# Performance work log

Hardware: AMD Instinct MI355X
Metric: run time of the kernel (lower is better)

The kernel has to match this reference:

```python
import jax, jax.numpy as jnp
import numpy as np

LEAK_VALUE = 0.1
B, N_ATOMS, IN_F, H, MAX_VAL, OUT_F = 256, 128, 128, 256, 6, 256


def gru(x, W_ih, W_hh, b_ih, b_hh):
    # x: [B, T, in]; W_ih: [3H, in]; W_hh: [3H, H]; gate order r,z,n (torch)
    Bb, T, _ = x.shape
    Hh = W_hh.shape[1]
    x_proj = jnp.einsum('bti,gi->btg', x, W_ih) + b_ih  # [B, T, 3H]

    def step(h, xp):
        gh = h @ W_hh.T + b_hh                      # [B, 3H]
        xr, xz, xn = jnp.split(xp, 3, axis=-1)
        hr, hz, hn = jnp.split(gh, 3, axis=-1)
        r = jax.nn.sigmoid(xr + hr)
        z = jax.nn.sigmoid(xz + hz)
        n = jnp.tanh(xn + r * hn)
        h_new = (1.0 - z) * n + z * h
        return h_new, h_new

    h0 = jnp.zeros((Bb, Hh), x.dtype)
    _, out = jax.lax.scan(step, h0, jnp.swapaxes(x_proj, 0, 1))  # [T, B, H]
    return jnp.swapaxes(out, 0, 1)  # [B, T, H]


def setup_inputs() -> dict:
    key = jax.random.key(0)
    ks = jax.random.split(key, 8)
    s = 0.05
    return {
        'x': jax.random.normal(ks[0], (B, N_ATOMS, IN_F), jnp.float32),
        'bonded_atoms': jax.random.randint(ks[1], (B, N_ATOMS, MAX_VAL), 0, N_ATOMS),
        'W_ih': jax.random.normal(ks[2], (3 * H, IN_F), jnp.float32) * s,
        'W_hh': jax.random.normal(ks[3], (3 * H, H), jnp.float32) * s,
        'b_ih': jax.random.normal(ks[4], (3 * H,), jnp.float32) * s,
        'b_hh': jax.random.normal(ks[5], (3 * H,), jnp.float32) * s,
        'W_fc': jax.random.normal(ks[6], (OUT_F, H * MAX_VAL), jnp.float32) * s,
        'b_fc': jax.random.normal(ks[7], (OUT_F,), jnp.float32) * s,
    }


def reference(x, bonded_atoms, W_ih, W_hh, b_ih, b_hh, W_fc, b_fc):
    rnn_out = gru(x, W_ih, W_hh, b_ih, b_hh)               # [B, N, H]
    batch_idx = jnp.arange(x.shape[0])[:, None, None]       # [B, 1, 1]
    fc_in = rnn_out[batch_idx, bonded_atoms]                # [B, N, V, H] gather
    fc_in = fc_in.reshape(x.shape[0], x.shape[1], -1)       # [B, N, V*H]
    out = fc_in @ W_fc.T + b_fc                             # [B, N, OUT_F]
    return jnp.where(out >= 0, out, LEAK_VALUE * out)
```

## Files before the change

kernel.cpp:

```cpp
#include <hip/hip_runtime.h>
#include <hip/hip_bf16.h>
#include <stdint.h>

typedef unsigned short u16;
typedef __bf16 bf16_t;
typedef bf16_t bf16x8 __attribute__((ext_vector_type(8)));
typedef u16    u16x8  __attribute__((ext_vector_type(8)));
typedef u16    u16x4  __attribute__((ext_vector_type(4)));
typedef float  f32x4  __attribute__((ext_vector_type(4)));

#define BSZ    256
#define NATOMS 128
#define INF    128
#define HH     256
#define H3     768
#define MAXV   6
#define OUTF   256
#define KFC    (HH * MAXV)
#define PLANE  8388608
#define HAP    264

__device__ __forceinline__ u16 f2bf(float f) {
  union { float f; unsigned u; } v; v.f = f;
  unsigned u = v.u;
  unsigned r = (u + 0x7FFFu + ((u >> 16) & 1u)) >> 16;
  return (u16)r;
}
__device__ __forceinline__ float bf2f(u16 h) {
  union { unsigned u; float f; } v; v.u = ((unsigned)h) << 16;
  return v.f;
}
__device__ __forceinline__ f32x4 mfma_bf16(u16x8 a, u16x8 b, f32x4 c) {
  return __builtin_amdgcn_mfma_f32_16x16x32_bf16(
      __builtin_bit_cast(bf16x8, a), __builtin_bit_cast(bf16x8, b), c, 0, 0, 0);
}
__device__ __forceinline__ float sel4(float a0, float a1, float a2, float a3, int q) {
  float t01 = (q & 1) ? a1 : a0;
  float t23 = (q & 1) ? a3 : a2;
  return (q & 2) ? t23 : t01;
}

#define NX4   1048576
#define C1    1048576
#define C2    1073152
#define C3    1122304
#define C4    1220608
__global__ void k_prep4(const float* __restrict__ x, const float* __restrict__ wih,
                        const float* __restrict__ whh, const float* __restrict__ wfc,
                        u16* __restrict__ xb, u16* __restrict__ wihb,
                        u16* __restrict__ whhb, u16* __restrict__ wfcb) {
  int i = blockIdx.x * 256 + threadIdx.x;
  const float* src; u16* dst; int j;
  if (i < C1)      { src = x;   dst = xb;   j = i; }
  else if (i < C2) { src = wih; dst = wihb; j = i - C1; }
  else if (i < C3) { src = whh; dst = whhb; j = i - C2; }
  else             { src = wfc; dst = wfcb; j = i - C3; }
  f32x4 v = *(const f32x4*)(src + (size_t)j * 4);
  u16x4 o;
#pragma unroll
  for (int k = 0; k < 4; k++) o[k] = f2bf(v[k]);
  *(u16x4*)(dst + (size_t)j * 4) = o;
}

__global__ __launch_bounds__(256) void k_xproj(const u16* __restrict__ X,
                                               const u16* __restrict__ W,
                                               const float* __restrict__ bias,
                                               const float* __restrict__ bhh,
                                               u16* __restrict__ out) {
  __shared__ __align__(16) u16 As[128][136];
  __shared__ __align__(16) u16 Bs[128][136];
  const int tid = threadIdx.x, lane = tid & 63, wid = tid >> 6;
  const int c16 = lane & 15, quad = lane >> 4;
  const int wm = (wid & 1) * 64, wn = (wid >> 1) * 64;
  const int bg = blockIdx.x >> 2, tg = blockIdx.x & 3;
  const int n0 = blockIdx.y * 128;

#pragma unroll
  for (int j = 0; j < 8; j++) {
    const int u = tid + j * 256, row = u >> 4, ch = u & 15;
    const int b = bg * 4 + (row & 3), t = tg * 32 + (row >> 2);
    *(u16x8*)&As[row][ch * 8] =
        *(const u16x8*)(X + ((size_t)b * 16384 + t * 128 + ch * 8));
    *(u16x8*)&Bs[row][ch * 8] =
        *(const u16x8*)(W + ((size_t)(n0 + row) * 128 + ch * 8));
  }
  __syncthreads();

  const f32x4 zero = {0.f, 0.f, 0.f, 0.f};
  f32x4 acc[4][4];
#pragma unroll
  for (int mi = 0; mi < 4; mi++)
#pragma unroll
    for (int ni = 0; ni < 4; ni++) acc[mi][ni] = zero;

#pragma unroll
  for (int kt = 0; kt < 4; kt++) {
    u16x8 af[4], bf[4];
#pragma unroll
    for (int mi = 0; mi < 4; mi++)
      af[mi] = *(const u16x8*)&As[wm + mi * 16 + c16][kt * 32 + quad * 8];
#pragma unroll
    for (int ni = 0; ni < 4; ni++)
      bf[ni] = *(const u16x8*)&Bs[wn + ni * 16 + c16][kt * 32 + quad * 8];
#pragma unroll
    for (int mi = 0; mi < 4; mi++)
#pragma unroll
      for (int ni = 0; ni < 4; ni++)
        acc[mi][ni] = mfma_bf16(af[mi], bf[ni], acc[mi][ni]);
  }

  const int bb = bg >> 2, mbh = bg & 3;
#pragma unroll
  for (int ni = 0; ni < 4; ni++) {
    const int n = n0 + wn + ni * 16 + c16;
    const int g = n >> 8, ww = (n >> 5) & 7, pp = (n >> 4) & 1, cc = n & 15;
    const float badd = bias[n] + (g < 2 ? bhh[n] : 0.f);
    u16* plane = out + (size_t)g * PLANE;
#pragma unroll
    for (int mi = 0; mi < 4; mi++) {
      const int t = tg * 32 + (wm >> 2) + mi * 4 + quad;
      u16x4 sv;
#pragma unroll
      for (int r_ = 0; r_ < 4; r_++) sv[r_] = f2bf(acc[mi][ni][r_] + badd);
      *(u16x4*)(plane + (((size_t)((bb * 128 + t) * 8 + ww)) << 9) +
                (mbh * 16 + cc) * 8 + pp * 4) = sv;
    }
  }
}

__global__ void __attribute__((amdgpu_flat_work_group_size(256, 256),
                               amdgpu_waves_per_eu(1, 1)))
k_gru(const u16* __restrict__ Whh, const float* __restrict__ bhh,
      const u16* __restrict__ xp2, u16* __restrict__ rnn) {
  __shared__ __align__(16) u16 hA[2][4 * HAP];
  const int tid = threadIdx.x, lane = tid & 63, w = tid >> 6;
  const int c = lane & 15, q = lane >> 4;
  const int b0 = blockIdx.x * 4;
  const int bb = blockIdx.x >> 2;
  const int Lq = (blockIdx.x & 3) * 16 + c;

  for (int i = tid; i < 2 * 4 * HAP; i += 256) ((u16*)hA)[i] = 0;

  u16x8 wf[12][8];
#pragma unroll
  for (int nt = 0; nt < 12; nt++)
#pragma unroll
    for (int kt = 0; kt < 8; kt++) {
      const int n = (nt >> 2) * 256 + w * 64 + (nt & 3) * 16 + c;
      wf[nt][kt] = *(const u16x8*)(Whh + (size_t)n * HH + kt * 32 + q * 8);
    }
#pragma unroll
  for (int nt = 0; nt < 12; nt++)
#pragma unroll
    for (int kt = 0; kt < 8; kt++) asm volatile("" : "+a"(wf[nt][kt]));

  const int col = w * 64 + q * 16 + c;
  const float bhhn = bhh[512 + col];
  float hreg[4] = {0.f, 0.f, 0.f, 0.f};

  const u16* gbase = xp2 + ((size_t)(bb * 128) * 8 + (w * 2 + (q >> 1))) * 512 +
                     (size_t)Lq * 8 + (q & 1) * 4;
  const int sl = lane & 31;
  u16* rnn_base = rnn + ((size_t)(b0 + w) * NATOMS) * HH + sl * 8;

  u16x4 xgn[3];
#pragma unroll
  for (int g = 0; g < 3; g++) xgn[g] = *(const u16x4*)(gbase + (size_t)g * PLANE);

  __syncthreads();

  const f32x4 zero4 = {0.f, 0.f, 0.f, 0.f};
#pragma unroll 1
  for (int t = 0; t < NATOMS; t++) {
    const u16* hc = hA[t & 1];
    u16* hnx = hA[(t + 1) & 1];

    if (t && lane < 32) {
      const u16x8 hv8 = *(const u16x8*)&hc[w * HAP + sl * 8];
      *(u16x8*)(rnn_base + (size_t)(t - 1) * HH) = hv8;
    }

    u16x4 xg[3];
#pragma unroll
    for (int g = 0; g < 3; g++) xg[g] = xgn[g];
    if (t < NATOMS - 1) {
      const u16* gp = gbase + (size_t)(t + 1) * 4096;
#pragma unroll
      for (int g = 0; g < 3; g++) xgn[g] = *(const u16x4*)(gp + (size_t)g * PLANE);
    }

    f32x4 acc[12];
#pragma unroll
    for (int nt = 0; nt < 12; nt++) acc[nt] = zero4;
#pragma unroll
    for (int kt = 0; kt < 8; kt++) {
      const u16x8 a = *(const u16x8*)&hc[(c & 3) * HAP + kt * 32 + q * 8];
#pragma unroll
      for (int nt = 0; nt < 12; nt++) acc[nt] = mfma_bf16(a, wf[nt][kt], acc[nt]);
    }

#pragma unroll
    for (int r_ = 0; r_ < 4; r_++) {
      const float Ar = sel4(acc[0][r_], acc[1][r_], acc[2][r_], acc[3][r_], q);
      const float Az = sel4(acc[4][r_], acc[5][r_], acc[6][r_], acc[7][r_], q);
      const float An = sel4(acc[8][r_], acc[9][r_], acc[10][r_], acc[11][r_], q);
      const float ar = Ar + bf2f(xg[0][r_]);
      const float az = Az + bf2f(xg[1][r_]);
      const float hn = An + bhhn;
      const float xn = bf2f(xg[2][r_]);
      const float rr = 1.f / (1.f + __expf(-ar));
      const float zz = 1.f / (1.f + __expf(-az));
      const float e  = __expf(2.f * (xn + rr * hn));
      const float nn = 1.f - 2.f / (e + 1.f);
      const float hv = nn + zz * (hreg[r_] - nn);
      hreg[r_] = hv;
      hnx[r_ * HAP + col] = f2bf(hv);
    }
    __syncthreads();
  }
  if (lane < 32) {
    const u16x8 hv8 = *(const u16x8*)&hA[0][w * HAP + sl * 8];
    *(u16x8*)(rnn_base + (size_t)(NATOMS - 1) * HH) = hv8;
  }
}

__global__ __launch_bounds__(256) void k_fc(const u16* __restrict__ rnn,
                                            const int* __restrict__ bonded,
                                            const u16* __restrict__ W,
                                            const float* __restrict__ bias,
                                            float* __restrict__ out) {
  __shared__ __align__(16) u16 As[128][72];
  __shared__ __align__(16) u16 Bs[128][72];
  __shared__ int ic[128][6];
  const int tid = threadIdx.x, lane = tid & 63, wid = tid >> 6;
  const int c16 = lane & 15, quad = lane >> 4;
  const int wNm = (wid & 1) * 64;
  const int wNa = (wid >> 1) * 64;
  const int bx = blockIdx.x, n0 = blockIdx.y * 128;

  for (int u = tid; u < 768; u += 256) {
    const int v = u >> 7, row = u & 127;
    ic[row][v] = bonded[(size_t)(bx * 128 + row) * MAXV + v];
  }
  __syncthreads();

  const f32x4 zero = {0.f, 0.f, 0.f, 0.f};
  f32x4 acc[4][4];
#pragma unroll
  for (int mi = 0; mi < 4; mi++)
#pragma unroll
    for (int ni = 0; ni < 4; ni++) acc[mi][ni] = zero;

  for (int it = 0; it < 24; it++) {
    const int kk = it * 64, v = kk >> 8, kr = kk & 255;
#pragma unroll
    for (int j = 0; j < 4; j++) {
      const int u = tid + j * 256, row = u >> 3, ch = u & 7;
      const int idx = ic[row][v];
      *(u16x8*)&As[row][ch * 8] =
          *(const u16x8*)(rnn + ((size_t)(bx * 128 + idx)) * HH + kr + ch * 8);
      *(u16x8*)&Bs[row][ch * 8] =
          *(const u16x8*)(W + (size_t)(n0 + row) * KFC + kk + ch * 8);
    }
    __syncthreads();
#pragma unroll
    for (int kt = 0; kt < 2; kt++) {
      u16x8 aw[4], ba[4];
#pragma unroll
      for (int mi = 0; mi < 4; mi++)
        aw[mi] = *(const u16x8*)&Bs[wNm + mi * 16 + c16][kt * 32 + quad * 8];
#pragma unroll
      for (int ni = 0; ni < 4; ni++)
        ba[ni] = *(const u16x8*)&As[wNa + ni * 16 + c16][kt * 32 + quad * 8];
#pragma unroll
      for (int mi = 0; mi < 4; mi++)
#pragma unroll
        for (int ni = 0; ni < 4; ni++)
          acc[mi][ni] = mfma_bf16(aw[mi], ba[ni], acc[mi][ni]);
    }
    __syncthreads();
  }

#pragma unroll
  for (int mi = 0; mi < 4; mi++) {
    const int n = n0 + wNm + mi * 16 + quad * 4;
    const f32x4 bv = *(const f32x4*)(bias + n);
#pragma unroll
    for (int ni = 0; ni < 4; ni++) {
      const int mm = bx * 128 + wNa + ni * 16 + c16;
      f32x4 vv;
#pragma unroll
      for (int r_ = 0; r_ < 4; r_++) {
        const float t = acc[mi][ni][r_] + bv[r_];
        vv[r_] = t >= 0.f ? t : 0.1f * t;
      }
      *(f32x4*)(out + (size_t)mm * OUTF + n) = vv;
    }
  }
}

extern "C" void kernel_launch(void* const* d_in, const int* in_sizes, int n_in,
                              void* d_out, int out_size, void* d_ws, size_t ws_size,
                              hipStream_t stream) {
  const float* x      = (const float*)d_in[0];
  const int*   bonded = (const int*)d_in[1];
  const float* Wih    = (const float*)d_in[2];
  const float* Whh    = (const float*)d_in[3];
  const float* bih    = (const float*)d_in[4];
  const float* bhh    = (const float*)d_in[5];
  const float* Wfc    = (const float*)d_in[6];
  const float* bfc    = (const float*)d_in[7];
  float* out = (float*)d_out;

  char* ws = (char*)d_ws;
  u16* xp2  = (u16*)(ws);
  u16* rnn  = (u16*)(ws + 50331648);
  u16* whhb = (u16*)(ws + 67108864);
  u16* wfcb = (u16*)(ws + 67502080);
  u16* xb   = (u16*)(ws + 68288512);
  u16* wihb = (u16*)(ws + 76677120);

  k_prep4<<<C4 / 256, 256, 0, stream>>>(x, Wih, Whh, Wfc, xb, wihb, whhb, wfcb);
  k_xproj<<<dim3(256, 6), 256, 0, stream>>>(xb, wihb, bih, bhh, xp2);
  k_gru<<<64, 256, 0, stream>>>(whhb, bhh, xp2, rnn);
  k_fc<<<dim3(256, 2), 256, 0, stream>>>(rnn, bonded, wfcb, bfc, out);
}
```

Before: 364.5 us.

## Deepen GRU gate prefetch to two steps and software-pipeline LDS h loads

The recurrent GRU loop now prefetches the input-projection gates two timesteps ahead using two alternating register buffers, with the loop unrolled by two. The LDS loads of the hidden-state A fragments are double-buffered across the k loop so the next load overlaps the current MFMAs, and the first MFMA takes a zero accumulator directly instead of a separate zero-init. __syncthreads is replaced by an explicit lgkmcnt wait plus s_barrier, so the barrier no longer waits on outstanding global (vmcnt) loads and the prefetches stay in flight across it. The aim is to hide global and LDS latency on the serial critical path, at the cost of more registers and a handwritten barrier.

```diff
diff --git a/kernel.cpp b/kernel.cpp
--- a/kernel.cpp
+++ b/kernel.cpp
@@ -163,15 +163,18 @@
   const int sl = lane & 31;
   u16* rnn_base = rnn + ((size_t)(b0 + w) * NATOMS) * HH + sl * 8;
 
-  u16x4 xgn[3];
-#pragma unroll
-  for (int g = 0; g < 3; g++) xgn[g] = *(const u16x4*)(gbase + (size_t)g * PLANE);
-
-  __syncthreads();
+  u16x4 xg0[3], xg1[3];
+#pragma unroll
+  for (int g = 0; g < 3; g++) xg0[g] = *(const u16x4*)(gbase + (size_t)g * PLANE);
+#pragma unroll
+  for (int g = 0; g < 3; g++) xg1[g] = *(const u16x4*)(gbase + 4096 + (size_t)g * PLANE);
+  const u16* gpre = gbase + 2 * 4096;
+
+  asm volatile("s_waitcnt lgkmcnt(0)\n\ts_barrier" ::: "memory");
 
   const f32x4 zero4 = {0.f, 0.f, 0.f, 0.f};
-#pragma unroll 1
-  for (int t = 0; t < NATOMS; t++) {
+
+  auto step = [&](const int t, u16x4 (&xgc)[3]) {
     const u16* hc = hA[t & 1];
     u16* hnx = hA[(t + 1) & 1];
 
@@ -182,21 +185,28 @@
 
     u16x4 xg[3];
 #pragma unroll
-    for (int g = 0; g < 3; g++) xg[g] = xgn[g];
-    if (t < NATOMS - 1) {
-      const u16* gp = gbase + (size_t)(t + 1) * 4096;
-#pragma unroll
-      for (int g = 0; g < 3; g++) xgn[g] = *(const u16x4*)(gp + (size_t)g * PLANE);
+    for (int g = 0; g < 3; g++) xg[g] = xgc[g];
+    if (t < NATOMS - 2) {
+#pragma unroll
+      for (int g = 0; g < 3; g++)
+        xgc[g] = *(const u16x4*)(gpre + (size_t)g * PLANE);
     }
 
     f32x4 acc[12];
-#pragma unroll
-    for (int nt = 0; nt < 12; nt++) acc[nt] = zero4;
+    u16x8 a0 = *(const u16x8*)&hc[(c & 3) * HAP + q * 8];
 #pragma unroll
     for (int kt = 0; kt < 8; kt++) {
-      const u16x8 a = *(const u16x8*)&hc[(c & 3) * HAP + kt * 32 + q * 8];
-#pragma unroll
-      for (int nt = 0; nt < 12; nt++) acc[nt] = mfma_bf16(a, wf[nt][kt], acc[nt]);
+      u16x8 a1;
+      if (kt < 7)
+        a1 = *(const u16x8*)&hc[(c & 3) * HAP + (kt + 1) * 32 + q * 8];
+      if (kt == 0) {
+#pragma unroll
+        for (int nt = 0; nt < 12; nt++) acc[nt] = mfma_bf16(a0, wf[nt][0], zero4);
+      } else {
+#pragma unroll
+        for (int nt = 0; nt < 12; nt++) acc[nt] = mfma_bf16(a0, wf[nt][kt], acc[nt]);
+      }
+      a0 = a1;
     }
 
 #pragma unroll
@@ -216,8 +226,18 @@
       hreg[r_] = hv;
       hnx[r_ * HAP + col] = f2bf(hv);
     }
-    __syncthreads();
-  }
+
+    asm volatile("s_waitcnt lgkmcnt(0)\n\ts_barrier" ::: "memory");
+  };
+
+#pragma unroll 1
+  for (int tt = 0; tt < NATOMS; tt += 2) {
+    step(tt, xg0);
+    gpre += 4096;
+    step(tt + 1, xg1);
+    gpre += 4096;
+  }
+
   if (lane < 32) {
     const u16x8 hv8 = *(const u16x8*)&hA[0][w * HAP + sl * 8];
     *(u16x8*)(rnn_base + (size_t)(NATOMS - 1) * HH) = hv8;
```

Measured after the change: 339.0 us. 7.0% less time.
